# Performance work log

Measured on AMD Instinct MI355X. Metric: run time of the kernel, lower is better.

## Reference

```python
import jax, jax.numpy as jnp
import numpy as np


def conv2d(x, w, b, pad=0):
    y = jax.lax.conv_general_dilated(x, w, (1, 1), [(pad, pad), (pad, pad)],
                                     dimension_numbers=('NCHW', 'OIHW', 'NCHW'))
    return y + b[None, :, None, None]


def leaky(x):
    return jnp.where(x >= 0, x, 0.1 * x)


def adaptive_pool3(x):
    # exact AdaptiveAvgPool2d((3,3)) when H,W divisible by 3
    B, C, H, W = x.shape
    return x.reshape(B, C, 3, H // 3, 3, W // 3).mean(axis=(3, 5))


def psf2otf(ker, H, W):
    # circularly shift PSF so its centre is at (0,0), then FFT (DWDN convention)
    B, C, kh, kw = ker.shape
    c = kh // 2 + 1
    psf = jnp.zeros((B, C, H, W), ker.dtype)
    psf = psf.at[:, :, :c, :c].set(ker[:, :, c - 1:, c - 1:])
    psf = psf.at[:, :, :c, -(c - 1):].set(ker[:, :, c - 1:, :c - 1])
    psf = psf.at[:, :, -(c - 1):, :c].set(ker[:, :, :c - 1, c - 1:])
    psf = psf.at[:, :, -(c - 1):, -(c - 1):].set(ker[:, :, :c - 1, :c - 1])
    return jnp.fft.fft2(psf)


def setup_inputs() -> dict:
    key = jax.random.key(0)
    ks = jax.random.split(key, 16)
    B, NF, C, H = 8, 64, 16, 246
    x = jax.random.normal(ks[0], (B, NF, H, H), jnp.float32)
    kernel = jax.random.uniform(ks[1], (B, 1, 21, 21), jnp.float32)
    kernel = kernel / kernel.sum(axis=(2, 3), keepdims=True)  # normalized blur PSF
    def w(k, shape):
        fan_in = shape[1] * shape[2] * shape[3]
        return jax.random.normal(k, shape, jnp.float32) / np.sqrt(fan_in)
    return {
        'x': x, 'kernel': kernel,
        'w_red': w(ks[2], (C, NF, 1, 1)), 'b_red': jnp.zeros((C,), jnp.float32),
        'w_g1': w(ks[3], (C, C, 3, 3)), 'b_g1': jnp.zeros((C,), jnp.float32),
        'w_g2': w(ks[4], (C, C, 3, 3)), 'b_g2': jnp.zeros((C,), jnp.float32),
        'w_g3': w(ks[5], (C, C, 3, 3)), 'b_g3': jnp.zeros((C,), jnp.float32),
        'w_g4': w(ks[6], (C, C, 1, 1)), 'b_g4': jnp.zeros((C,), jnp.float32),
        'w_exp': w(ks[7], (NF, C, 1, 1)), 'b_exp': jnp.zeros((NF,), jnp.float32),
    }


def reference(x, kernel, w_red, b_red, w_g1, b_g1, w_g2, b_g2, w_g3, b_g3,
              w_g4, b_g4, w_exp, b_exp):
    cls_feats = conv2d(x, w_red, b_red)                      # [B,C,H,W]
    h = leaky(conv2d(cls_feats, w_g1, b_g1))                 # valid 3x3 convs
    h = leaky(conv2d(h, w_g2, b_g2))
    h = conv2d(h, w_g3, b_g3)
    h = adaptive_pool3(h)                                    # [B,C,3,3]
    kernel_P = jnp.exp(conv2d(h, w_g4, b_g4))
    kernel_P = kernel_P - kernel_P.mean(axis=(2, 3), keepdims=True)

    ks_ = kernel.shape[-1]
    fp = jnp.pad(cls_feats, ((0, 0), (0, 0), (ks_, ks_), (ks_, ks_)), mode='edge')
    Hp, Wp = fp.shape[2], fp.shape[3]
    # batched Wiener deconvolution over all channels at once (replaces per-channel loop)
    Kf = psf2otf(kernel, Hp, Wp)                             # [B,1,Hp,Wp] complex
    Pf = psf2otf(kernel_P, Hp, Wp)                           # [B,C,Hp,Wp] complex
    denom = Kf.real ** 2 + Kf.imag ** 2 + Pf.real ** 2 + Pf.imag ** 2
    inv_ker = jnp.conj(Kf) / denom                           # conj(K)/(|K|^2+|P|^2)
    deblur = jnp.fft.ifft2(inv_ker * jnp.fft.fft2(fp)).real
    clear = deblur[:, :, ks_:-ks_, ks_:-ks_]
    return conv2d(clear, w_exp, b_exp)
```

## Files before the change

### kernel.cpp

```cpp
#include <hip/hip_runtime.h>
#include <hip/hip_bf16.h>

__device__ inline float2 cadd(float2 a, float2 b){ return make_float2(a.x+b.x, a.y+b.y); }
__device__ inline float2 csub(float2 a, float2 b){ return make_float2(a.x-b.x, a.y-b.y); }
__device__ inline float2 cmul(float2 a, float2 b){
    return make_float2(fmaf(a.x,b.x,-a.y*b.y), fmaf(a.x,b.y,a.y*b.x));
}

#define NPIX 60516
#define NFFT 288
#define NFFT2 82944

template<bool INV>
__device__ inline void bf4(float2 a0, float2 a1, float2 a2, float2 a3,
                           float2& b0, float2& b1, float2& b2, float2& b3) {
    float2 t0=cadd(a0,a2), t1=csub(a0,a2), t2=cadd(a1,a3), t3=csub(a1,a3);
    b0=cadd(t0,t2); b2=csub(t0,t2);
    if (!INV) { b1=make_float2(t1.x+t3.y, t1.y-t3.x); b3=make_float2(t1.x-t3.y, t1.y+t3.x); }
    else      { b1=make_float2(t1.x-t3.y, t1.y+t3.x); b3=make_float2(t1.x+t3.y, t1.y-t3.x); }
}
template<bool INV>
__device__ inline void bf3(float2 a0, float2 a1, float2 a2,
                           float2& b0, float2& b1, float2& b2) {
    const float d = INV ? 0.8660254037844386f : -0.8660254037844386f;
    float2 tt=cadd(a1,a2), u=csub(a1,a2);
    b0=cadd(a0,tt);
    b1=make_float2(a0.x-0.5f*tt.x - d*u.y, a0.y-0.5f*tt.y + d*u.x);
    b2=make_float2(a0.x-0.5f*tt.x + d*u.y, a0.y-0.5f*tt.y - d*u.x);
}

template<bool INV>
__device__ inline void fft288_row(float2*& X, float2*& Y, int lane, const float2* __restrict__ tw) {
    auto TW = [&](int k) { float2 v = tw[k]; if (INV) v.y = -v.y; return v; };
    for (int p = lane; p < 72; p += 64) {
        float2 b0,b1,b2,b3;
        bf4<INV>(X[p], X[p+72], X[p+144], X[p+216], b0,b1,b2,b3);
        Y[4*p]=b0; Y[4*p+1]=cmul(b1,TW(p)); Y[4*p+2]=cmul(b2,TW(2*p)); Y[4*p+3]=cmul(b3,TW(3*p));
    }
    __syncthreads(); { float2* t=X; X=Y; Y=t; }
    for (int it = lane; it < 72; it += 64) {
        int p = it>>2, q = it&3, i0 = q+4*p;
        float2 b0,b1,b2,b3;
        bf4<INV>(X[i0], X[i0+72], X[i0+144], X[i0+216], b0,b1,b2,b3);
        int o = q+16*p;
        Y[o]=b0; Y[o+4]=cmul(b1,TW(4*p)); Y[o+8]=cmul(b2,TW(8*p)); Y[o+12]=cmul(b3,TW(12*p));
    }
    __syncthreads(); { float2* t=X; X=Y; Y=t; }
    for (int it = lane; it < 144; it += 64) {
        int p = it>>4, q = it&15, i0 = q+16*p;
        float2 a0=X[i0], a1=X[i0+144];
        int o = q+32*p;
        Y[o]=cadd(a0,a1); Y[o+16]=cmul(csub(a0,a1),TW(16*p));
    }
    __syncthreads(); { float2* t=X; X=Y; Y=t; }
    for (int it = lane; it < 96; it += 64) {
        int p = it>>5, q = it&31, i0 = q+32*p;
        float2 b0,b1,b2;
        bf3<INV>(X[i0], X[i0+96], X[i0+192], b0,b1,b2);
        int o = q+96*p;
        Y[o]=b0; Y[o+32]=cmul(b1,TW(32*p)); Y[o+64]=cmul(b2,TW(64*p));
    }
    __syncthreads(); { float2* t=X; X=Y; Y=t; }
    for (int q = lane; q < 96; q += 64) {
        float2 b0,b1,b2;
        bf3<INV>(X[q], X[q+96], X[q+192], b0,b1,b2);
        Y[q]=b0; Y[q+96]=b1; Y[q+192]=b2;
    }
    __syncthreads(); { float2* t=X; X=Y; Y=t; }
}

__global__ void k_tw(float2* tw) {
    int k = threadIdx.x;
    if (k < NFFT) {
        double ang = -2.0 * 3.14159265358979323846 * (double)k / (double)NFFT;
        tw[k] = make_float2((float)cos(ang), (float)sin(ang));
    }
}

__global__ __launch_bounds__(256) void k_conv1x1_red(const float* __restrict__ x,
        const float* __restrict__ w, const float* __restrict__ bias, float* __restrict__ out) {
    int idx = blockIdx.x * 256 + threadIdx.x;
    if (idx >= 8 * NPIX) return;
    int b = idx / NPIX, p = idx % NPIX;
    const float* xb = x + (size_t)b * 64 * NPIX + p;
    float acc[16];
    #pragma unroll
    for (int co = 0; co < 16; co++) acc[co] = bias[co];
    for (int ci = 0; ci < 64; ci++) {
        float v = xb[(size_t)ci * NPIX];
        #pragma unroll
        for (int co = 0; co < 16; co++) acc[co] = fmaf(w[co*64+ci], v, acc[co]);
    }
    float* ob = out + (size_t)b * 16 * NPIX + p;
    #pragma unroll
    for (int co = 0; co < 16; co++) ob[(size_t)co*NPIX] = acc[co];
}

template<int HIN, bool LEAKY>
__global__ __launch_bounds__(256) void k_conv3x3(const float* __restrict__ in,
        const float* __restrict__ w, const float* __restrict__ bias, float* __restrict__ out) {
    const int HOUT = HIN - 2;
    const int GX = (HOUT + 3) / 4;
    int idx = blockIdx.x * 256 + threadIdx.x;
    if (idx >= 8 * HOUT * GX) return;
    int b  = idx / (HOUT * GX);
    int r  = idx % (HOUT * GX);
    int oy = r / GX;
    int ox0 = (r % GX) * 4;

    float acc[16][4];
    #pragma unroll
    for (int co = 0; co < 16; co++) {
        float bb = bias[co];
        #pragma unroll
        for (int px = 0; px < 4; px++) acc[co][px] = bb;
    }
    const float* ib = in + (size_t)b * 16 * HIN * HIN + (size_t)oy * HIN;
    for (int ci = 0; ci < 16; ci++) {
        const float* ic = ib + (size_t)ci * HIN * HIN;
        #pragma unroll
        for (int ky = 0; ky < 3; ky++) {
            float in6[6];
            #pragma unroll
            for (int j = 0; j < 6; j++) {
                int xx = ox0 + j;
                if (HOUT % 4 != 0) { if (xx > HIN - 1) xx = HIN - 1; }
                in6[j] = ic[ky * HIN + xx];
            }
            #pragma unroll
            for (int kx = 0; kx < 3; kx++) {
                #pragma unroll
                for (int co = 0; co < 16; co++) {
                    float wv = w[co*144 + ci*9 + ky*3 + kx];
                    #pragma unroll
                    for (int px = 0; px < 4; px++)
                        acc[co][px] = fmaf(wv, in6[px + kx], acc[co][px]);
                }
            }
        }
    }
    float* ob = out + (size_t)b * 16 * HOUT * HOUT + (size_t)oy * HOUT + ox0;
    #pragma unroll
    for (int co = 0; co < 16; co++) {
        #pragma unroll
        for (int px = 0; px < 4; px++) {
            if (HOUT % 4 == 0 || ox0 + px < HOUT) {
                float v = acc[co][px];
                if (LEAKY) v = (v >= 0.f) ? v : 0.1f * v;
                ob[(size_t)co * HOUT * HOUT + px] = v;
            }
        }
    }
}

__global__ __launch_bounds__(256) void k_pool3(const float* __restrict__ in, float* __restrict__ out) {
    int bc = blockIdx.x;
    int cell = bc % 9, ch = bc / 9;
    int by = cell / 3, bx = cell % 3;
    const float* base = in + (size_t)ch * 240*240 + (size_t)by*80*240 + bx*80;
    float s = 0.f;
    for (int i = threadIdx.x; i < 6400; i += 256) {
        int r = i / 80, c = i % 80;
        s += base[r*240 + c];
    }
    __shared__ float red[256];
    red[threadIdx.x] = s; __syncthreads();
    for (int st = 128; st > 0; st >>= 1) {
        if (threadIdx.x < st) red[threadIdx.x] += red[threadIdx.x+st];
        __syncthreads();
    }
    if (threadIdx.x == 0) out[bc] = red[0] * (1.f/6400.f);
}

__global__ void k_kernelP(const float* __restrict__ pooled, const float* __restrict__ w,
                          const float* __restrict__ bias, float* __restrict__ out) {
    int b = blockIdx.x / 16, co = blockIdx.x % 16;
    __shared__ float vals[9];
    int t = threadIdx.x;
    if (t < 9) {
        float a = bias[co];
        for (int ci = 0; ci < 16; ci++) a += pooled[(b*16+ci)*9 + t] * w[co*16+ci];
        vals[t] = expf(a);
    }
    __syncthreads();
    if (t < 9) {
        float m = 0.f;
        #pragma unroll
        for (int i = 0; i < 9; i++) m += vals[i];
        m *= (1.f/9.f);
        out[(b*16+co)*9 + t] = vals[t] - m;
    }
}

__global__ __launch_bounds__(256) void k_psfK(const float* __restrict__ ker, float2* __restrict__ Kf) {
    int idx = blockIdx.x*256 + threadIdx.x;
    if (idx >= 8*NFFT2) return;
    int pos = idx % NFFT2, b = idx / NFFT2;
    int y = pos / NFFT, x = pos % NFFT;
    int ry = (y < 11) ? y+10 : ((y >= 278) ? y-278 : -1);
    int rx = (x < 11) ? x+10 : ((x >= 278) ? x-278 : -1);
    float v = (ry >= 0 && rx >= 0) ? ker[b*441 + ry*21 + rx] : 0.f;
    Kf[idx] = make_float2(v, 0.f);
}

template<bool INV>
__global__ __launch_bounds__(256) void k_fft_rows(float2* __restrict__ M, const float2* __restrict__ tw) {
    __shared__ float2 A[4][NFFT];
    __shared__ float2 B[4][NFFT];
    int t = threadIdx.x, w = t >> 6, lane = t & 63;
    size_t row = (size_t)blockIdx.x*4 + w;
    float2* X = A[w]; float2* Y = B[w];
    float2* s = M + row*NFFT;
    for (int j = lane; j < NFFT; j += 64) X[j] = s[j];
    __syncthreads();
    fft288_row<INV>(X, Y, lane, tw);
    for (int j = lane; j < NFFT; j += 64) s[j] = X[j];
}

__global__ __launch_bounds__(256) void k_fft_rows_pad(const float* __restrict__ cls,
        float2* __restrict__ Z, const float2* __restrict__ tw) {
    __shared__ float2 A[4][NFFT];
    __shared__ float2 B[4][NFFT];
    int t = threadIdx.x, w = t >> 6, lane = t & 63;
    size_t row = (size_t)blockIdx.x*4 + w;
    int pc = (int)(row / NFFT), y = (int)(row % NFFT);
    int iy = min(max(y-21, 0), 245);
    const float* c0 = cls + (size_t)(2*pc)*NPIX + (size_t)iy*246;
    float2* X = A[w]; float2* Y = B[w];
    for (int j = lane; j < NFFT; j += 64) {
        int ix = min(max(j-21, 0), 245);
        X[j] = make_float2(c0[ix], c0[NPIX+ix]);
    }
    __syncthreads();
    fft288_row<false>(X, Y, lane, tw);
    float2* d = Z + row*NFFT;
    for (int j = lane; j < NFFT; j += 64) d[j] = X[j];
}

__global__ __launch_bounds__(256) void k_ifft_rows_crop(const float2* __restrict__ Z,
        float* __restrict__ clear, const float2* __restrict__ tw) {
    __shared__ float2 A[4][NFFT];
    __shared__ float2 B[4][NFFT];
    int t = threadIdx.x, w = t >> 6, lane = t & 63;
    int ch = blockIdx.x / 62;
    int rseq = (blockIdx.x % 62)*4 + w;
    bool valid = rseq < 246;
    int y = rseq + 21;
    float2* X = A[w]; float2* Y = B[w];
    if (valid) {
        const float2* s = Z + (size_t)ch*NFFT2 + (size_t)y*NFFT;
        for (int j = lane; j < NFFT; j += 64) X[j] = s[j];
    }
    __syncthreads();
    fft288_row<true>(X, Y, lane, tw);
    if (valid) {
        const float sc = 1.0f / 82944.0f;
        float* o0 = clear + (size_t)(2*ch)*NPIX + (size_t)rseq*246;
        for (int j = lane; j < 246; j += 64) {
            float2 v = X[j+21];
            o0[j]        = v.x * sc;
            o0[NPIX + j] = v.y * sc;
        }
    }
}

template<bool INV>
__global__ __launch_bounds__(256) void k_fft_cols(float2* __restrict__ M, const float2* __restrict__ tw) {
    __shared__ float2 Abuf[NFFT*9];
    __shared__ float2 Bbuf[NFFT*9];
    int t = threadIdx.x, c = t & 7, w = t >> 3;
    int ch = blockIdx.x / 36, cg = blockIdx.x % 36;
    float2* base = M + (size_t)ch * NFFT2 + cg*8 + c;
    float2* X = Abuf; float2* Y = Bbuf;
    for (int r = w; r < NFFT; r += 32) X[r*9 + c] = base[(size_t)r * NFFT];
    __syncthreads();
    auto TW = [&](int k) { float2 v = tw[k]; if (INV) v.y = -v.y; return v; };
    for (int p = w; p < 72; p += 32) {
        float2 b0,b1,b2,b3;
        bf4<INV>(X[p*9+c], X[(p+72)*9+c], X[(p+144)*9+c], X[(p+216)*9+c], b0,b1,b2,b3);
        Y[(4*p)*9+c]=b0; Y[(4*p+1)*9+c]=cmul(b1,TW(p));
        Y[(4*p+2)*9+c]=cmul(b2,TW(2*p)); Y[(4*p+3)*9+c]=cmul(b3,TW(3*p));
    }
    __syncthreads(); { float2* tp=X; X=Y; Y=tp; }
    for (int it = w; it < 72; it += 32) {
        int p = it>>2, q = it&3, i0 = q+4*p;
        float2 b0,b1,b2,b3;
        bf4<INV>(X[i0*9+c], X[(i0+72)*9+c], X[(i0+144)*9+c], X[(i0+216)*9+c], b0,b1,b2,b3);
        int o = q+16*p;
        Y[o*9+c]=b0; Y[(o+4)*9+c]=cmul(b1,TW(4*p));
        Y[(o+8)*9+c]=cmul(b2,TW(8*p)); Y[(o+12)*9+c]=cmul(b3,TW(12*p));
    }
    __syncthreads(); { float2* tp=X; X=Y; Y=tp; }
    for (int it = w; it < 144; it += 32) {
        int p = it>>4, q = it&15, i0 = q+16*p;
        float2 a0=X[i0*9+c], a1=X[(i0+144)*9+c];
        int o = q+32*p;
        Y[o*9+c]=cadd(a0,a1); Y[(o+16)*9+c]=cmul(csub(a0,a1),TW(16*p));
    }
    __syncthreads(); { float2* tp=X; X=Y; Y=tp; }
    for (int it = w; it < 96; it += 32) {
        int p = it>>5, q = it&31, i0 = q+32*p;
        float2 b0,b1,b2;
        bf3<INV>(X[i0*9+c], X[(i0+96)*9+c], X[(i0+192)*9+c], b0,b1,b2);
        int o = q+96*p;
        Y[o*9+c]=b0; Y[(o+32)*9+c]=cmul(b1,TW(32*p)); Y[(o+64)*9+c]=cmul(b2,TW(64*p));
    }
    __syncthreads(); { float2* tp=X; X=Y; Y=tp; }
    for (int q = w; q < 96; q += 32) {
        float2 b0,b1,b2;
        bf3<INV>(X[q*9+c], X[(q+96)*9+c], X[(q+192)*9+c], b0,b1,b2);
        Y[q*9+c]=b0; Y[(q+96)*9+c]=b1; Y[(q+192)*9+c]=b2;
    }
    __syncthreads(); { float2* tp=X; X=Y; Y=tp; }
    for (int r = w; r < NFFT; r += 32) base[(size_t)r * NFFT] = X[r*9 + c];
}

__global__ __launch_bounds__(256) void k_invker(float2* __restrict__ Z, const float* __restrict__ kP,
        const float2* __restrict__ Kf, const float2* __restrict__ tw) {
    int pc = blockIdx.x / 164;
    int q  = (blockIdx.x % 164) * 256 + threadIdx.x;
    if (q >= 145*288) return;
    int yh = q / 288, x = q % 288;
    bool self = false;
    if (yh == 0 || yh == 144) {
        if (x == 0 || x == 144) self = true;
        else if (x > 144) return;
    }
    int y = yh;
    int my = (NFFT - y) % NFFT;
    int mx = (NFFT - x) % NFFT;
    size_t basez = (size_t)pc * NFFT2;
    int pos = y*NFFT + x, mpos = my*NFFT + mx;
    float2 zk = Z[basez + pos];
    float2 zm = self ? zk : Z[basez + mpos];
    int b = pc >> 3;
    float2 K = Kf[(size_t)b*NFFT2 + pos];
    float2 wy = tw[y], wx = tw[x];
    const float* pA = kP + (size_t)(2*pc)*9;
    const float* pB = pA + 9;
    auto otf3 = [&](const float* p9) {
        float2 R0 = make_float2(p9[1] + (p9[0]+p9[2])*wx.x, (p9[2]-p9[0])*wx.y);
        float2 R1 = make_float2(p9[4] + (p9[3]+p9[5])*wx.x, (p9[5]-p9[3])*wx.y);
        float2 R2 = make_float2(p9[7] + (p9[6]+p9[8])*wx.x, (p9[8]-p9[6])*wx.y);
        float2 P;
        P.x = R1.x + wy.x*(R0.x+R2.x) - wy.y*(R2.y-R0.y);
        P.y = R1.y + wy.x*(R0.y+R2.y) + wy.y*(R2.x-R0.x);
        return P;
    };
    float2 Pa = otf3(pA);
    float2 Pb = otf3(pB);
    float2 A_ = make_float2(0.5f*(zk.x+zm.x),  0.5f*(zk.y-zm.y));
    float2 B_ = make_float2(0.5f*(zk.y+zm.y), -0.5f*(zk.x-zm.x));
    float kk = K.x*K.x + K.y*K.y;
    float ra = 1.0f / (kk + Pa.x*Pa.x + Pa.y*Pa.y);
    float rb = 1.0f / (kk + Pb.x*Pb.x + Pb.y*Pb.y);
    float2 Ha = make_float2(K.x*ra, -K.y*ra);
    float2 Hb = make_float2(K.x*rb, -K.y*rb);
    float2 Fa = cmul(Ha, A_);
    float2 Fb = cmul(Hb, B_);
    Z[basez + pos] = make_float2(Fa.x - Fb.y, Fa.y + Fb.x);
    if (!self)
        Z[basez + mpos] = make_float2(Fa.x + Fb.y, Fb.x - Fa.y);
}

__global__ __launch_bounds__(256) void k_conv1x1_exp(const float* __restrict__ clear,
        const float* __restrict__ w, const float* __restrict__ bias, float* __restrict__ out) {
    int idx = blockIdx.x * 256 + threadIdx.x;
    if (idx >= 8 * NPIX) return;
    int b = idx / NPIX, p = idx % NPIX;
    const float* cb = clear + (size_t)b * 16 * NPIX + p;
    float v[16];
    #pragma unroll
    for (int ci = 0; ci < 16; ci++) v[ci] = cb[(size_t)ci*NPIX];
    float* ob = out + (size_t)b * 64 * NPIX + p;
    #pragma unroll
    for (int co = 0; co < 64; co++) {
        float a = bias[co];
        #pragma unroll
        for (int ci = 0; ci < 16; ci++) a = fmaf(w[co*16+ci], v[ci], a);
        ob[(size_t)co*NPIX] = a;
    }
}

extern "C" void kernel_launch(void* const* d_in, const int* in_sizes, int n_in,
                              void* d_out, int out_size, void* d_ws, size_t ws_size,
                              hipStream_t stream) {
    const float* x     = (const float*)d_in[0];
    const float* ker   = (const float*)d_in[1];
    const float* w_red = (const float*)d_in[2];
    const float* b_red = (const float*)d_in[3];
    const float* w_g1  = (const float*)d_in[4];
    const float* b_g1  = (const float*)d_in[5];
    const float* w_g2  = (const float*)d_in[6];
    const float* b_g2  = (const float*)d_in[7];
    const float* w_g3  = (const float*)d_in[8];
    const float* b_g3  = (const float*)d_in[9];
    const float* w_g4  = (const float*)d_in[10];
    const float* b_g4  = (const float*)d_in[11];
    const float* w_exp = (const float*)d_in[12];
    const float* b_exp = (const float*)d_in[13];
    float* out = (float*)d_out;

    char* ws = (char*)d_ws;
    size_t off = 0;
    auto alloc = [&](size_t bytes) -> char* {
        char* p = ws + off; off += (bytes + 255) & ~(size_t)255; return p;
    };
    float*  cls    = (float*) alloc(7746048ull * 4);
    float2* Z      = (float2*)alloc((size_t)64 * NFFT2 * 8);
    float*  clear  = (float*) alloc(7746048ull * 4);
    float2* Kf     = (float2*)alloc((size_t)8 * NFFT2 * 8);
    float*  pooled = (float*) alloc(1152 * 4);
    float*  kP     = (float*) alloc(1152 * 4);
    float2* tw     = (float2*)alloc(288 * 8);
    float*  ha     = (float*)Z;
    float*  hb     = (float*)clear;

    k_tw<<<1, 320, 0, stream>>>(tw);
    k_conv1x1_red<<<1892, 256, 0, stream>>>(x, w_red, b_red, cls);
    k_conv3x3<246, true ><<<466, 256, 0, stream>>>(cls, w_g1, b_g1, ha);
    k_conv3x3<244, true ><<<462, 256, 0, stream>>>(ha,  w_g2, b_g2, hb);
    k_conv3x3<242, false><<<450, 256, 0, stream>>>(hb,  w_g3, b_g3, ha);
    k_pool3<<<1152, 256, 0, stream>>>(ha, pooled);
    k_kernelP<<<128, 64, 0, stream>>>(pooled, w_g4, b_g4, kP);

    k_psfK<<<2592, 256, 0, stream>>>(ker, Kf);
    k_fft_rows<false><<<576, 256, 0, stream>>>(Kf, tw);
    k_fft_cols<false><<<288, 256, 0, stream>>>(Kf, tw);

    k_fft_rows_pad<<<4608, 256, 0, stream>>>(cls, Z, tw);
    k_fft_cols<false><<<2304, 256, 0, stream>>>(Z, tw);

    k_invker<<<10496, 256, 0, stream>>>(Z, kP, Kf, tw);

    k_fft_cols<true><<<2304, 256, 0, stream>>>(Z, tw);
    k_ifft_rows_crop<<<3968, 256, 0, stream>>>(Z, clear, tw);

    k_conv1x1_exp<<<1892, 256, 0, stream>>>(clear, w_exp, b_exp, out);
}
```

Baseline: 364.9 us.

## Fuse column FFTs with Wiener filter, fuse conv3 with pooling, fuse iFFT with expand conv

Merges the forward column FFT, the Wiener inverse-kernel multiply and the inverse column FFT into one kernel. Columns are paired with their conjugate mirrors inside a block, and the PSF OTF is stored transposed so it can be read per column. The last 3x3 conv now reduces straight into the pooled sums with shared and global atomics, so the full feature map is never written. The inverse row FFT is fused with the 1x1 expansion conv, which removes the intermediate 'clear' buffer and several full-size global round trips. The cost is heavier kernels with more shared memory and registers, and atomics that make the pooled sum order nondeterministic.

```diff
diff --git a/kernel.cpp b/kernel.cpp
--- a/kernel.cpp
+++ b/kernel.cpp
@@ -69,12 +69,57 @@
     __syncthreads(); { float2* t=X; X=Y; Y=t; }
 }
 
-__global__ void k_tw(float2* tw) {
-    int k = threadIdx.x;
-    if (k < NFFT) {
-        double ang = -2.0 * 3.14159265358979323846 * (double)k / (double)NFFT;
-        tw[k] = make_float2((float)cos(ang), (float)sin(ang));
-    }
+template<bool INV>
+__device__ inline void fft288_s9(float2*& X, float2*& Y, int w, int c, const float2* __restrict__ tw) {
+    auto TW = [&](int k) { float2 v = tw[k]; if (INV) v.y = -v.y; return v; };
+    #define SIX(i) ((i)*9 + c)
+    for (int p = w; p < 72; p += 32) {
+        float2 b0,b1,b2,b3;
+        bf4<INV>(X[SIX(p)], X[SIX(p+72)], X[SIX(p+144)], X[SIX(p+216)], b0,b1,b2,b3);
+        Y[SIX(4*p)]=b0; Y[SIX(4*p+1)]=cmul(b1,TW(p));
+        Y[SIX(4*p+2)]=cmul(b2,TW(2*p)); Y[SIX(4*p+3)]=cmul(b3,TW(3*p));
+    }
+    __syncthreads(); { float2* t=X; X=Y; Y=t; }
+    for (int it = w; it < 72; it += 32) {
+        int p = it>>2, q = it&3, i0 = q+4*p;
+        float2 b0,b1,b2,b3;
+        bf4<INV>(X[SIX(i0)], X[SIX(i0+72)], X[SIX(i0+144)], X[SIX(i0+216)], b0,b1,b2,b3);
+        int o = q+16*p;
+        Y[SIX(o)]=b0; Y[SIX(o+4)]=cmul(b1,TW(4*p));
+        Y[SIX(o+8)]=cmul(b2,TW(8*p)); Y[SIX(o+12)]=cmul(b3,TW(12*p));
+    }
+    __syncthreads(); { float2* t=X; X=Y; Y=t; }
+    for (int it = w; it < 144; it += 32) {
+        int p = it>>4, q = it&15, i0 = q+16*p;
+        float2 a0=X[SIX(i0)], a1=X[SIX(i0+144)];
+        int o = q+32*p;
+        Y[SIX(o)]=cadd(a0,a1); Y[SIX(o+16)]=cmul(csub(a0,a1),TW(16*p));
+    }
+    __syncthreads(); { float2* t=X; X=Y; Y=t; }
+    for (int it = w; it < 96; it += 32) {
+        int p = it>>5, q = it&31, i0 = q+32*p;
+        float2 b0,b1,b2;
+        bf3<INV>(X[SIX(i0)], X[SIX(i0+96)], X[SIX(i0+192)], b0,b1,b2);
+        int o = q+96*p;
+        Y[SIX(o)]=b0; Y[SIX(o+32)]=cmul(b1,TW(32*p)); Y[SIX(o+64)]=cmul(b2,TW(64*p));
+    }
+    __syncthreads(); { float2* t=X; X=Y; Y=t; }
+    for (int q = w; q < 96; q += 32) {
+        float2 b0,b1,b2;
+        bf3<INV>(X[SIX(q)], X[SIX(q+96)], X[SIX(q+192)], b0,b1,b2);
+        Y[SIX(q)]=b0; Y[SIX(q+96)]=b1; Y[SIX(q+192)]=b2;
+    }
+    __syncthreads(); { float2* t=X; X=Y; Y=t; }
+    #undef SIX
+}
+
+__global__ void k_tw(float2* tw, float* pooled) {
+    int t = threadIdx.x;
+    if (t < NFFT) {
+        double ang = -2.0 * 3.14159265358979323846 * (double)t / (double)NFFT;
+        tw[t] = make_float2((float)cos(ang), (float)sin(ang));
+    }
+    for (int i = t; i < 1152; i += 320) pooled[i] = 0.f;
 }
 
 __global__ __launch_bounds__(256) void k_conv1x1_red(const float* __restrict__ x,
@@ -153,23 +198,58 @@
     }
 }
 
-__global__ __launch_bounds__(256) void k_pool3(const float* __restrict__ in, float* __restrict__ out) {
-    int bc = blockIdx.x;
-    int cell = bc % 9, ch = bc / 9;
-    int by = cell / 3, bx = cell % 3;
-    const float* base = in + (size_t)ch * 240*240 + (size_t)by*80*240 + bx*80;
-    float s = 0.f;
-    for (int i = threadIdx.x; i < 6400; i += 256) {
-        int r = i / 80, c = i % 80;
-        s += base[r*240 + c];
-    }
-    __shared__ float red[256];
-    red[threadIdx.x] = s; __syncthreads();
-    for (int st = 128; st > 0; st >>= 1) {
-        if (threadIdx.x < st) red[threadIdx.x] += red[threadIdx.x+st];
-        __syncthreads();
-    }
-    if (threadIdx.x == 0) out[bc] = red[0] * (1.f/6400.f);
+__global__ __launch_bounds__(256) void k_conv3x3_pool(const float* __restrict__ in,
+        const float* __restrict__ w, const float* __restrict__ bias, float* __restrict__ pooled) {
+    const int HIN = 242, GX = 60;
+    __shared__ float cs[144];
+    int t = threadIdx.x;
+    int b = blockIdx.x / 57;
+    int r = (blockIdx.x % 57) * 256 + t;
+    bool valid = r < 14400;
+    float partial[16];
+    int cell = 0;
+    if (valid) {
+        int oy = r / GX, ox0 = (r % GX) * 4;
+        cell = (oy / 80) * 3 + (ox0 / 80);
+        float acc[16][4];
+        #pragma unroll
+        for (int co = 0; co < 16; co++) {
+            float bb = bias[co];
+            #pragma unroll
+            for (int px = 0; px < 4; px++) acc[co][px] = bb;
+        }
+        const float* ib = in + (size_t)b * 16 * HIN * HIN + (size_t)oy * HIN;
+        for (int ci = 0; ci < 16; ci++) {
+            const float* ic = ib + (size_t)ci * HIN * HIN;
+            #pragma unroll
+            for (int ky = 0; ky < 3; ky++) {
+                float in6[6];
+                #pragma unroll
+                for (int j = 0; j < 6; j++) in6[j] = ic[ky * HIN + ox0 + j];
+                #pragma unroll
+                for (int kx = 0; kx < 3; kx++) {
+                    #pragma unroll
+                    for (int co = 0; co < 16; co++) {
+                        float wv = w[co*144 + ci*9 + ky*3 + kx];
+                        #pragma unroll
+                        for (int px = 0; px < 4; px++)
+                            acc[co][px] = fmaf(wv, in6[px + kx], acc[co][px]);
+                    }
+                }
+            }
+        }
+        #pragma unroll
+        for (int co = 0; co < 16; co++)
+            partial[co] = (acc[co][0] + acc[co][1]) + (acc[co][2] + acc[co][3]);
+    }
+    if (t < 144) cs[t] = 0.f;
+    __syncthreads();
+    if (valid) {
+        #pragma unroll
+        for (int co = 0; co < 16; co++) atomicAdd(&cs[co*9 + cell], partial[co]);
+    }
+    __syncthreads();
+    if (t < 144) atomicAdd(&pooled[b*144 + t], cs[t]);
 }
 
 __global__ void k_kernelP(const float* __restrict__ pooled, const float* __restrict__ w,
@@ -178,9 +258,9 @@
     __shared__ float vals[9];
     int t = threadIdx.x;
     if (t < 9) {
-        float a = bias[co];
+        float a = 0.f;
         for (int ci = 0; ci < 16; ci++) a += pooled[(b*16+ci)*9 + t] * w[co*16+ci];
-        vals[t] = expf(a);
+        vals[t] = expf(bias[co] + a * (1.f/6400.f));
     }
     __syncthreads();
     if (t < 9) {
@@ -192,15 +272,15 @@
     }
 }
 
-__global__ __launch_bounds__(256) void k_psfK(const float* __restrict__ ker, float2* __restrict__ Kf) {
+__global__ __launch_bounds__(256) void k_psfKT(const float* __restrict__ ker, float2* __restrict__ KfT) {
     int idx = blockIdx.x*256 + threadIdx.x;
     if (idx >= 8*NFFT2) return;
     int pos = idx % NFFT2, b = idx / NFFT2;
-    int y = pos / NFFT, x = pos % NFFT;
-    int ry = (y < 11) ? y+10 : ((y >= 278) ? y-278 : -1);
-    int rx = (x < 11) ? x+10 : ((x >= 278) ? x-278 : -1);
-    float v = (ry >= 0 && rx >= 0) ? ker[b*441 + ry*21 + rx] : 0.f;
-    Kf[idx] = make_float2(v, 0.f);
+    int u = pos / NFFT, v = pos % NFFT;
+    int ry = (v < 11) ? v+10 : ((v >= 278) ? v-278 : -1);
+    int rx = (u < 11) ? u+10 : ((u >= 278) ? u-278 : -1);
+    float val = (ry >= 0 && rx >= 0) ? ker[b*441 + ry*21 + rx] : 0.f;
+    KfT[idx] = make_float2(val, 0.f);
 }
 
 template<bool INV>
@@ -215,6 +295,20 @@
     __syncthreads();
     fft288_row<INV>(X, Y, lane, tw);
     for (int j = lane; j < NFFT; j += 64) s[j] = X[j];
+}
+
+template<bool INV>
+__global__ __launch_bounds__(256) void k_fft_cols(float2* __restrict__ M, const float2* __restrict__ tw) {
+    __shared__ float2 Abuf[NFFT*9];
+    __shared__ float2 Bbuf[NFFT*9];
+    int t = threadIdx.x, c = t & 7, w = t >> 3;
+    int ch = blockIdx.x / 36, cg = blockIdx.x % 36;
+    float2* base = M + (size_t)ch * NFFT2 + cg*8 + c;
+    float2* X = Abuf; float2* Y = Bbuf;
+    for (int r = w; r < NFFT; r += 32) X[r*9 + c] = base[(size_t)r * NFFT];
+    __syncthreads();
+    fft288_s9<INV>(X, Y, w, c, tw);
+    for (int r = w; r < NFFT; r += 32) base[(size_t)r * NFFT] = X[r*9 + c];
 }
 
 __global__ __launch_bounds__(256) void k_fft_rows_pad(const float* __restrict__ cls,
@@ -237,148 +331,97 @@
     for (int j = lane; j < NFFT; j += 64) d[j] = X[j];
 }
 
-__global__ __launch_bounds__(256) void k_ifft_rows_crop(const float2* __restrict__ Z,
-        float* __restrict__ clear, const float2* __restrict__ tw) {
-    __shared__ float2 A[4][NFFT];
-    __shared__ float2 B[4][NFFT];
-    int t = threadIdx.x, w = t >> 6, lane = t & 63;
-    int ch = blockIdx.x / 62;
-    int rseq = (blockIdx.x % 62)*4 + w;
-    bool valid = rseq < 246;
-    int y = rseq + 21;
-    float2* X = A[w]; float2* Y = B[w];
-    if (valid) {
-        const float2* s = Z + (size_t)ch*NFFT2 + (size_t)y*NFFT;
-        for (int j = lane; j < NFFT; j += 64) X[j] = s[j];
-    }
-    __syncthreads();
-    fft288_row<true>(X, Y, lane, tw);
-    if (valid) {
-        const float sc = 1.0f / 82944.0f;
-        float* o0 = clear + (size_t)(2*ch)*NPIX + (size_t)rseq*246;
-        for (int j = lane; j < 246; j += 64) {
-            float2 v = X[j+21];
-            o0[j]        = v.x * sc;
-            o0[NPIX + j] = v.y * sc;
-        }
-    }
-}
-
-template<bool INV>
-__global__ __launch_bounds__(256) void k_fft_cols(float2* __restrict__ M, const float2* __restrict__ tw) {
+__global__ __launch_bounds__(256) void k_fft_cols_filter(float2* __restrict__ Z,
+        const float2* __restrict__ KfT, const float* __restrict__ kP, const float2* __restrict__ tw) {
     __shared__ float2 Abuf[NFFT*9];
     __shared__ float2 Bbuf[NFFT*9];
     int t = threadIdx.x, c = t & 7, w = t >> 3;
-    int ch = blockIdx.x / 36, cg = blockIdx.x % 36;
-    float2* base = M + (size_t)ch * NFFT2 + cg*8 + c;
+    int ch = blockIdx.x / 36, g = blockIdx.x % 36;
+    int colc, pi;
+    if (g == 0) {
+        colc = (c < 4) ? c : (c == 4 ? 144 : 292 - c);
+        pi   = (c == 0 || c == 4) ? c : (c < 4 ? c + 4 : c - 4);
+    } else {
+        colc = (c < 4) ? (4*g + c) : (288 - 4*g - (c - 4));
+        pi   = c ^ 4;
+    }
+    float2* zb = Z + (size_t)ch * NFFT2 + colc;
     float2* X = Abuf; float2* Y = Bbuf;
-    for (int r = w; r < NFFT; r += 32) X[r*9 + c] = base[(size_t)r * NFFT];
-    __syncthreads();
-    auto TW = [&](int k) { float2 v = tw[k]; if (INV) v.y = -v.y; return v; };
-    for (int p = w; p < 72; p += 32) {
-        float2 b0,b1,b2,b3;
-        bf4<INV>(X[p*9+c], X[(p+72)*9+c], X[(p+144)*9+c], X[(p+216)*9+c], b0,b1,b2,b3);
-        Y[(4*p)*9+c]=b0; Y[(4*p+1)*9+c]=cmul(b1,TW(p));
-        Y[(4*p+2)*9+c]=cmul(b2,TW(2*p)); Y[(4*p+3)*9+c]=cmul(b3,TW(3*p));
-    }
-    __syncthreads(); { float2* tp=X; X=Y; Y=tp; }
-    for (int it = w; it < 72; it += 32) {
-        int p = it>>2, q = it&3, i0 = q+4*p;
-        float2 b0,b1,b2,b3;
-        bf4<INV>(X[i0*9+c], X[(i0+72)*9+c], X[(i0+144)*9+c], X[(i0+216)*9+c], b0,b1,b2,b3);
-        int o = q+16*p;
-        Y[o*9+c]=b0; Y[(o+4)*9+c]=cmul(b1,TW(4*p));
-        Y[(o+8)*9+c]=cmul(b2,TW(8*p)); Y[(o+12)*9+c]=cmul(b3,TW(12*p));
-    }
-    __syncthreads(); { float2* tp=X; X=Y; Y=tp; }
-    for (int it = w; it < 144; it += 32) {
-        int p = it>>4, q = it&15, i0 = q+16*p;
-        float2 a0=X[i0*9+c], a1=X[(i0+144)*9+c];
-        int o = q+32*p;
-        Y[o*9+c]=cadd(a0,a1); Y[(o+16)*9+c]=cmul(csub(a0,a1),TW(16*p));
-    }
-    __syncthreads(); { float2* tp=X; X=Y; Y=tp; }
-    for (int it = w; it < 96; it += 32) {
-        int p = it>>5, q = it&31, i0 = q+32*p;
-        float2 b0,b1,b2;
-        bf3<INV>(X[i0*9+c], X[(i0+96)*9+c], X[(i0+192)*9+c], b0,b1,b2);
-        int o = q+96*p;
-        Y[o*9+c]=b0; Y[(o+32)*9+c]=cmul(b1,TW(32*p)); Y[(o+64)*9+c]=cmul(b2,TW(64*p));
-    }
-    __syncthreads(); { float2* tp=X; X=Y; Y=tp; }
-    for (int q = w; q < 96; q += 32) {
-        float2 b0,b1,b2;
-        bf3<INV>(X[q*9+c], X[(q+96)*9+c], X[(q+192)*9+c], b0,b1,b2);
-        Y[q*9+c]=b0; Y[(q+96)*9+c]=b1; Y[(q+192)*9+c]=b2;
-    }
-    __syncthreads(); { float2* tp=X; X=Y; Y=tp; }
-    for (int r = w; r < NFFT; r += 32) base[(size_t)r * NFFT] = X[r*9 + c];
-}
-
-__global__ __launch_bounds__(256) void k_invker(float2* __restrict__ Z, const float* __restrict__ kP,
-        const float2* __restrict__ Kf, const float2* __restrict__ tw) {
-    int pc = blockIdx.x / 164;
-    int q  = (blockIdx.x % 164) * 256 + threadIdx.x;
-    if (q >= 145*288) return;
-    int yh = q / 288, x = q % 288;
-    bool self = false;
-    if (yh == 0 || yh == 144) {
-        if (x == 0 || x == 144) self = true;
-        else if (x > 144) return;
-    }
-    int y = yh;
-    int my = (NFFT - y) % NFFT;
-    int mx = (NFFT - x) % NFFT;
-    size_t basez = (size_t)pc * NFFT2;
-    int pos = y*NFFT + x, mpos = my*NFFT + mx;
-    float2 zk = Z[basez + pos];
-    float2 zm = self ? zk : Z[basez + mpos];
-    int b = pc >> 3;
-    float2 K = Kf[(size_t)b*NFFT2 + pos];
-    float2 wy = tw[y], wx = tw[x];
-    const float* pA = kP + (size_t)(2*pc)*9;
-    const float* pB = pA + 9;
-    auto otf3 = [&](const float* p9) {
-        float2 R0 = make_float2(p9[1] + (p9[0]+p9[2])*wx.x, (p9[2]-p9[0])*wx.y);
-        float2 R1 = make_float2(p9[4] + (p9[3]+p9[5])*wx.x, (p9[5]-p9[3])*wx.y);
-        float2 R2 = make_float2(p9[7] + (p9[6]+p9[8])*wx.x, (p9[8]-p9[6])*wx.y);
-        float2 P;
-        P.x = R1.x + wy.x*(R0.x+R2.x) - wy.y*(R2.y-R0.y);
-        P.y = R1.y + wy.x*(R0.y+R2.y) + wy.y*(R2.x-R0.x);
-        return P;
-    };
-    float2 Pa = otf3(pA);
-    float2 Pb = otf3(pB);
-    float2 A_ = make_float2(0.5f*(zk.x+zm.x),  0.5f*(zk.y-zm.y));
-    float2 B_ = make_float2(0.5f*(zk.y+zm.y), -0.5f*(zk.x-zm.x));
-    float kk = K.x*K.x + K.y*K.y;
-    float ra = 1.0f / (kk + Pa.x*Pa.x + Pa.y*Pa.y);
-    float rb = 1.0f / (kk + Pb.x*Pb.x + Pb.y*Pb.y);
-    float2 Ha = make_float2(K.x*ra, -K.y*ra);
-    float2 Hb = make_float2(K.x*rb, -K.y*rb);
-    float2 Fa = cmul(Ha, A_);
-    float2 Fb = cmul(Hb, B_);
-    Z[basez + pos] = make_float2(Fa.x - Fb.y, Fa.y + Fb.x);
-    if (!self)
-        Z[basez + mpos] = make_float2(Fa.x + Fb.y, Fb.x - Fa.y);
-}
-
-__global__ __launch_bounds__(256) void k_conv1x1_exp(const float* __restrict__ clear,
-        const float* __restrict__ w, const float* __restrict__ bias, float* __restrict__ out) {
-    int idx = blockIdx.x * 256 + threadIdx.x;
-    if (idx >= 8 * NPIX) return;
-    int b = idx / NPIX, p = idx % NPIX;
-    const float* cb = clear + (size_t)b * 16 * NPIX + p;
-    float v[16];
-    #pragma unroll
-    for (int ci = 0; ci < 16; ci++) v[ci] = cb[(size_t)ci*NPIX];
-    float* ob = out + (size_t)b * 64 * NPIX + p;
-    #pragma unroll
-    for (int co = 0; co < 64; co++) {
-        float a = bias[co];
-        #pragma unroll
-        for (int ci = 0; ci < 16; ci++) a = fmaf(w[co*16+ci], v[ci], a);
-        ob[(size_t)co*NPIX] = a;
+    for (int r = w; r < NFFT; r += 32) X[r*9 + c] = zb[(size_t)r * NFFT];
+    __syncthreads();
+    fft288_s9<false>(X, Y, w, c, tw);
+    {
+        int b = ch >> 3;
+        const float* pA = kP + (size_t)(2*ch)*9;
+        const float* pB = pA + 9;
+        float2 wx = tw[colc];
+        const float2* Kcol = KfT + (size_t)b*NFFT2 + (size_t)colc*NFFT;
+        for (int y = w; y < NFFT; y += 32) {
+            int my = (y == 0) ? 0 : NFFT - y;
+            float2 zk = X[y*9 + c];
+            float2 zm = X[my*9 + pi];
+            float2 K  = Kcol[y];
+            float2 wy = tw[y];
+            auto otf3 = [&](const float* p9) {
+                float2 R0 = make_float2(p9[1] + (p9[0]+p9[2])*wx.x, (p9[2]-p9[0])*wx.y);
+                float2 R1 = make_float2(p9[4] + (p9[3]+p9[5])*wx.x, (p9[5]-p9[3])*wx.y);
+                float2 R2 = make_float2(p9[7] + (p9[6]+p9[8])*wx.x, (p9[8]-p9[6])*wx.y);
+                float2 P;
+                P.x = R1.x + wy.x*(R0.x+R2.x) - wy.y*(R2.y-R0.y);
+                P.y = R1.y + wy.x*(R0.y+R2.y) + wy.y*(R2.x-R0.x);
+                return P;
+            };
+            float2 Pa = otf3(pA);
+            float2 Pb = otf3(pB);
+            float2 A_ = make_float2(0.5f*(zk.x+zm.x),  0.5f*(zk.y-zm.y));
+            float2 B_ = make_float2(0.5f*(zk.y+zm.y), -0.5f*(zk.x-zm.x));
+            float kk = K.x*K.x + K.y*K.y;
+            float ra = 1.0f / (kk + Pa.x*Pa.x + Pa.y*Pa.y);
+            float rb = 1.0f / (kk + Pb.x*Pb.x + Pb.y*Pb.y);
+            float2 Ha = make_float2(K.x*ra, -K.y*ra);
+            float2 Hb = make_float2(K.x*rb, -K.y*rb);
+            float2 Fa = cmul(Ha, A_);
+            float2 Fb = cmul(Hb, B_);
+            Y[y*9 + c] = make_float2(Fa.x - Fb.y, Fa.y + Fb.x);
+        }
+    }
+    __syncthreads();
+    { float2* tp = X; X = Y; Y = tp; }
+    fft288_s9<true>(X, Y, w, c, tw);
+    for (int r = w; r < NFFT; r += 32) zb[(size_t)r * NFFT] = X[r*9 + c];
+}
+
+__global__ __launch_bounds__(256) void k_ifft_rows_conv(const float2* __restrict__ Z,
+        const float* __restrict__ w_exp, const float* __restrict__ b_exp,
+        float* __restrict__ out, const float2* __restrict__ tw) {
+    __shared__ float2 Abuf[NFFT*9];
+    __shared__ float2 Bbuf[NFFT*9];
+    int t = threadIdx.x, c = t & 7, w = t >> 3;
+    int b = blockIdx.x / 246;
+    int rseq = blockIdx.x % 246;
+    int y = rseq + 21;
+    const float2* s = Z + (size_t)(b*8 + c) * NFFT2 + (size_t)y * NFFT;
+    float2* X = Abuf; float2* Y = Bbuf;
+    for (int j = w; j < NFFT; j += 32) X[j*9 + c] = s[j];
+    __syncthreads();
+    fft288_s9<true>(X, Y, w, c, tw);
+    if (t < 246) {
+        const float sc = 1.0f / 82944.0f;
+        float v[16];
+        #pragma unroll
+        for (int h = 0; h < 8; h++) {
+            float2 z = X[(t + 21)*9 + h];
+            v[2*h]   = z.x * sc;
+            v[2*h+1] = z.y * sc;
+        }
+        float* ob = out + (size_t)b * 64 * NPIX + (size_t)rseq * 246 + t;
+        #pragma unroll
+        for (int co = 0; co < 64; co++) {
+            float a = b_exp[co];
+            #pragma unroll
+            for (int ci = 0; ci < 16; ci++) a = fmaf(w_exp[co*16+ci], v[ci], a);
+            ob[(size_t)co * NPIX] = a;
+        }
     }
 }
 
@@ -408,33 +451,27 @@
     };
     float*  cls    = (float*) alloc(7746048ull * 4);
     float2* Z      = (float2*)alloc((size_t)64 * NFFT2 * 8);
-    float*  clear  = (float*) alloc(7746048ull * 4);
-    float2* Kf     = (float2*)alloc((size_t)8 * NFFT2 * 8);
+    float*  hb     = (float*) alloc(7495712ull * 4);
+    float2* KfT    = (float2*)alloc((size_t)8 * NFFT2 * 8);
     float*  pooled = (float*) alloc(1152 * 4);
     float*  kP     = (float*) alloc(1152 * 4);
     float2* tw     = (float2*)alloc(288 * 8);
     float*  ha     = (float*)Z;
-    float*  hb     = (float*)clear;
-
-    k_tw<<<1, 320, 0, stream>>>(tw);
+
+    k_tw<<<1, 320, 0, stream>>>(tw, pooled);
     k_conv1x1_red<<<1892, 256, 0, stream>>>(x, w_red, b_red, cls);
     k_conv3x3<246, true ><<<466, 256, 0, stream>>>(cls, w_g1, b_g1, ha);
     k_conv3x3<244, true ><<<462, 256, 0, stream>>>(ha,  w_g2, b_g2, hb);
-    k_conv3x3<242, false><<<450, 256, 0, stream>>>(hb,  w_g3, b_g3, ha);
-    k_pool3<<<1152, 256, 0, stream>>>(ha, pooled);
+    k_conv3x3_pool<<<456, 256, 0, stream>>>(hb, w_g3, b_g3, pooled);
     k_kernelP<<<128, 64, 0, stream>>>(pooled, w_g4, b_g4, kP);
 
-    k_psfK<<<2592, 256, 0, stream>>>(ker, Kf);
-    k_fft_rows<false><<<576, 256, 0, stream>>>(Kf, tw);
-    k_fft_cols<false><<<288, 256, 0, stream>>>(Kf, tw);
+    k_psfKT<<<2592, 256, 0, stream>>>(ker, KfT);
+    k_fft_rows<false><<<576, 256, 0, stream>>>(KfT, tw);
+    k_fft_cols<false><<<288, 256, 0, stream>>>(KfT, tw);
 
     k_fft_rows_pad<<<4608, 256, 0, stream>>>(cls, Z, tw);
-    k_fft_cols<false><<<2304, 256, 0, stream>>>(Z, tw);
-
-    k_invker<<<10496, 256, 0, stream>>>(Z, kP, Kf, tw);
-
-    k_fft_cols<true><<<2304, 256, 0, stream>>>(Z, tw);
-    k_ifft_rows_crop<<<3968, 256, 0, stream>>>(Z, clear, tw);
-
-    k_conv1x1_exp<<<1892, 256, 0, stream>>>(clear, w_exp, b_exp, out);
-}
+
+    k_fft_cols_filter<<<2304, 256, 0, stream>>>(Z, KfT, kP, tw);
+
+    k_ifft_rows_conv<<<1968, 256, 0, stream>>>(Z, w_exp, b_exp, out, tw);
+}
```

After: 357.7 us. 1.02x faster.
